# Kernel optimization log

Hardware: AMD Instinct MI355X
Metric: run time of the kernel (lower is better)

Reference implementation:

```python
import jax, jax.numpy as jnp
import numpy as np

B, T, C = 64, 256, 1024
N_HEAD, HEAD_SIZE, KV_RANK = 16, 64, 128
BLOCK_SIZE = 256


def setup_inputs() -> dict:
    key = jax.random.key(0)
    ks = jax.random.split(key, 5)
    HD = N_HEAD * HEAD_SIZE
    # weights stored (in, out) so y = x @ W  (equivalent to torch Linear x @ W.T)
    def init(k, shape):
        fan_in = shape[0]
        bound = 1.0 / np.sqrt(fan_in)
        return jax.random.uniform(k, shape, jnp.float32, -bound, bound)
    return {
        "x": jax.random.normal(ks[0], (B, T, C), jnp.float32),
        "w_kv_down": init(ks[1], (C, KV_RANK)),
        "w_kv_up": init(ks[2], (KV_RANK, 2 * HD)),
        "w_q": init(ks[3], (C, HD)),
        "w_out": init(ks[4], (HD, C)),
    }


def reference(x, w_kv_down, w_kv_up, w_q, w_out):
    Bx, Tx, Cx = x.shape
    HD = N_HEAD * HEAD_SIZE
    latent_kv = x @ w_kv_down                          # [B,T,r]
    kv = latent_kv @ w_kv_up                            # [B,T,2*H*D]
    k, v = kv[..., :HD], kv[..., HD:]
    k = k.reshape(Bx, Tx, N_HEAD, HEAD_SIZE)           # [B,T,H,D]
    v = v.reshape(Bx, Tx, N_HEAD, HEAD_SIZE)
    q = (x @ w_q).reshape(Bx, Tx, N_HEAD, HEAD_SIZE)
    scale = HEAD_SIZE ** -0.5
    att = jnp.einsum("bqhd,bkhd->bhqk", q, k) * scale  # [B,H,T,T]
    causal = jnp.tril(jnp.ones((Tx, Tx), dtype=bool))
    att = jnp.where(causal, att, -jnp.inf)
    att = jax.nn.softmax(att, axis=-1)                  # dropout = identity (eval)
    y = jnp.einsum("bhqk,bkhd->bqhd", att, v)          # [B,T,H,D]
    y = y.reshape(Bx, Tx, HD)
    return y @ w_out
```

## Files before the change

### kernel.cpp

```cpp
#include <hip/hip_runtime.h>
#include <hip/hip_bf16.h>
#include <cstdint>
#include <cstddef>

typedef short short8 __attribute__((ext_vector_type(8)));
typedef float floatx4 __attribute__((ext_vector_type(4)));
typedef float floatx16 __attribute__((ext_vector_type(16)));
typedef unsigned short u16;
typedef unsigned int u32;

__device__ __forceinline__ u16 f2bf(float f) {
    __hip_bfloat16 h = __float2bfloat16(f);
    return __builtin_bit_cast(u16, h);
}

__device__ __forceinline__ void gload_lds16(const void* g, void* l) {
    __builtin_amdgcn_global_load_lds(
        (const __attribute__((address_space(1))) void*)g,
        (__attribute__((address_space(3))) void*)l, 16, 0, 0);
}

__global__ __launch_bounds__(256) void prep(const float* __restrict__ x, u16* __restrict__ xb,
                                            const float* __restrict__ wq, const float* __restrict__ wkvd,
                                            const float* __restrict__ wkvu, const float* __restrict__ wo,
                                            u16* __restrict__ wql_t, u16* __restrict__ wkvu_t,
                                            u16* __restrict__ wo_t) {
    const int b = blockIdx.x;
    if (b < 2048) {
        const int n4 = 16384 * 1024 / 4;
        for (int i = b * 256 + threadIdx.x; i < n4; i += 2048 * 256) {
            float4 v = ((const float4*)x)[i];
            ushort4 o;
            o.x = f2bf(v.x); o.y = f2bf(v.y); o.z = f2bf(v.z); o.w = f2bf(v.w);
            ((ushort4*)xb)[i] = o;
        }
    } else {
        __shared__ float tile[32][33];
        const float* W; u16* Wt; int K, N, lb;
        if (b < 3072)      { W = wq;   Wt = wql_t;                       K = 1024; N = 1024; lb = b - 2048; }
        else if (b < 3200) { W = wkvd; Wt = wql_t + (size_t)1024 * 1024; K = 1024; N = 128;  lb = b - 3072; }
        else if (b < 3456) { W = wkvu; Wt = wkvu_t;                      K = 128;  N = 2048; lb = b - 3200; }
        else               { W = wo;   Wt = wo_t;                        K = 1024; N = 1024; lb = b - 3456; }
        const int nb = N / 32;
        const int n0 = (lb % nb) * 32, k0 = (lb / nb) * 32;
        const int tx = threadIdx.x & 31, ty = threadIdx.x >> 5;
        #pragma unroll
        for (int i = 0; i < 32; i += 8)
            tile[ty + i][tx] = W[(size_t)(k0 + ty + i) * N + n0 + tx];
        __syncthreads();
        #pragma unroll
        for (int i = 0; i < 32; i += 8)
            Wt[(size_t)(n0 + ty + i) * K + k0 + tx] = f2bf(tile[tx][ty + i]);
    }
}

template <int MODE>
__global__ __launch_bounds__(256, 4) void gemm_bt64(const u16* __restrict__ A, const u16* __restrict__ Bt,
                                                    void* __restrict__ C, int M, int N, int K, int ncols) {
    __shared__ __align__(16) u16 As[128 * 64];
    __shared__ __align__(16) u16 Bs[128 * 64];
    const int tid = threadIdx.x;
    const int lane = tid & 63, wid = tid >> 6;
    const int wr = wid >> 1, wc = wid & 1;
    const int l15 = lane & 15, hi = lane >> 4;

    const int nwg = gridDim.x, q8 = nwg >> 3;
    const int wg = (blockIdx.x & 7) * q8 + (blockIdx.x >> 3);
    const int m0 = (wg / ncols) * 128, n0 = (wg % ncols) * 128;

    const u16* Ab = A + (size_t)m0 * K;
    const u16* Bb = Bt + (size_t)n0 * K;

    u32 soff[4];
    #pragma unroll
    for (int l = 0; l < 4; l++) {
        int p = l * 256 + tid, c = p ^ ((p >> 3) & 7);
        soff[l] = (u32)((c >> 3) * K + (c & 7) * 8);
    }

    int afo[4][2], bfo[4][2];
    #pragma unroll
    for (int i = 0; i < 4; i++) {
        #pragma unroll
        for (int ks = 0; ks < 2; ks++) {
            int ra = wr * 64 + i * 16 + l15;
            afo[i][ks] = ((ra * 8 + ks * 4 + hi) ^ (ra & 7)) * 8;
            int rb = wc * 64 + i * 16 + l15;
            bfo[i][ks] = ((rb * 8 + ks * 4 + hi) ^ (rb & 7)) * 8;
        }
    }

    floatx4 acc[4][4] = {};

    for (int k0 = 0; k0 < K; k0 += 64) {
        #pragma unroll
        for (int l = 0; l < 4; l++)
            gload_lds16(Ab + soff[l] + k0, As + (size_t)(l * 256 + wid * 64) * 8);
        #pragma unroll
        for (int l = 0; l < 4; l++)
            gload_lds16(Bb + soff[l] + k0, Bs + (size_t)(l * 256 + wid * 64) * 8);
        __syncthreads();
        #pragma unroll
        for (int ks = 0; ks < 2; ks++) {
            short8 af[4], bf[4];
            #pragma unroll
            for (int i = 0; i < 4; i++) af[i] = *(const short8*)&As[afo[i][ks]];
            #pragma unroll
            for (int j = 0; j < 4; j++) bf[j] = *(const short8*)&Bs[bfo[j][ks]];
            #pragma unroll
            for (int i = 0; i < 4; i++) {
                #pragma unroll
                for (int j = 0; j < 4; j++)
                    acc[i][j] = __builtin_amdgcn_mfma_f32_16x16x32_bf16(af[i], bf[j], acc[i][j], 0, 0, 0);
            }
        }
        __syncthreads();
    }

    const int cr = hi * 4, cc = l15;
    #pragma unroll
    for (int i = 0; i < 4; i++) {
        #pragma unroll
        for (int j = 0; j < 4; j++) {
            int row = m0 + wr * 64 + i * 16 + cr;
            int col = n0 + wc * 64 + j * 16 + cc;
            #pragma unroll
            for (int r = 0; r < 4; r++) {
                float v = acc[i][j][r];
                int rr = row + r;
                if (MODE == 0) {
                    ((float*)C)[(size_t)rr * N + col] = v;
                } else {
                    if (col < 1024) {
                        int h = col >> 6, dd = col & 63;
                        ((u16*)C)[(((size_t)(rr >> 8) * 16 + h) * 256 + (rr & 255)) * 64 + dd] = f2bf(v);
                    } else {
                        u16* lat = (u16*)C + (size_t)16384 * 1024;
                        lat[(size_t)rr * 128 + (col - 1024)] = f2bf(v);
                    }
                }
            }
        }
    }
}

__global__ __launch_bounds__(256, 2) void attn_fused(const u16* __restrict__ Qh, const u16* __restrict__ Lat,
                                                     const u16* __restrict__ Wu, u16* __restrict__ Y) {
    constexpr int T = 256, HD = 1024;
    constexpr int VS = 264;
    __shared__ __align__(16) u16 Ks[256 * 64];
    __shared__ __align__(16) u16 Vt[64 * VS];

    const int tid = threadIdx.x, lane = tid & 63, wid = tid >> 6;
    const int bh = blockIdx.x;
    const int b = bh >> 4, h = bh & 15;
    const size_t base = (size_t)bh * (T * 64);
    const size_t baseY = (size_t)b * T * HD + (size_t)h * 64;

    const int qcol = lane & 31, hi2 = lane >> 5;

    {
        const u16* latb = Lat + (size_t)b * 256 * 128;
        const u16* wK = Wu + (size_t)(h * 64) * 128;
        const u16* wV = Wu + (size_t)(1024 + h * 64) * 128;

        #pragma unroll
        for (int i = 0; i < 4; i++) {
            const int tt = wid * 2 + (i >> 1), dt = i & 1;
            const u16* lp = &latb[(size_t)(tt * 32 + qcol) * 128 + hi2 * 8];
            const u16* kp = &wK[(size_t)(dt * 32 + qcol) * 128 + hi2 * 8];
            const u16* vp = &wV[(size_t)(dt * 32 + qcol) * 128 + hi2 * 8];
            floatx16 ck = {0}, cv = {0};
            #pragma unroll
            for (int ks = 0; ks < 8; ks++) {
                short8 lf = *(const short8*)&lp[ks * 16];
                short8 kf = *(const short8*)&kp[ks * 16];
                short8 vf = *(const short8*)&vp[ks * 16];
                ck = __builtin_amdgcn_mfma_f32_32x32x16_bf16(lf, kf, ck, 0, 0, 0);
                cv = __builtin_amdgcn_mfma_f32_32x32x16_bf16(vf, lf, cv, 0, 0, 0);
            }
            const int dK = dt * 32 + qcol;
            const int tV = tt * 32 + qcol;
            #pragma unroll
            for (int r = 0; r < 16; r++) {
                const int rloc = (r & 3) + 8 * (r >> 2) + 4 * hi2;
                const int t = tt * 32 + rloc;
                const int xt = (t & 7) ^ ((t >> 3) & 3);
                Ks[t * 64 + (((dK >> 3) ^ xt) << 3) + (dK & 7)] = f2bf(ck[r]);
                Vt[(dt * 32 + rloc) * VS + tV] = f2bf(cv[r]);
            }
        }
    }
    __syncthreads();

    const float c_exp = 0.125f * 1.44269504088896f;
    const u16* qbase = Qh + base;
    const u16* vrow0 = &Vt[qcol * VS];
    const u16* vrow1 = &Vt[(qcol + 32) * VS];

    #pragma unroll 1
    for (int half = 0; half < 2; half++) {
        const int qb = half ? (7 - wid) : wid;

        short8 qf[4];
        {
            const u16* qp = &qbase[(size_t)(qb * 32 + qcol) * 64 + hi2 * 8];
            #pragma unroll
            for (int i = 0; i < 4; i++) qf[i] = *(const short8*)&qp[i * 16];
        }

        floatx16 y0 = {0}, y1 = {0};
        float lsum = 0.f;

        for (int kt = 0; kt <= qb; kt++) {
            const int tK = kt * 32 + qcol;
            const int xt = (tK & 7) ^ ((tK >> 3) & 3);
            const u16* kp = &Ks[tK * 64];
            floatx16 s = {0};
            #pragma unroll
            for (int i = 0; i < 4; i++) {
                short8 kf = *(const short8*)&kp[((i * 2 + hi2) ^ xt) << 3];
                s = __builtin_amdgcn_mfma_f32_32x32x16_bf16(kf, qf[i], s, 0, 0, 0);
            }

            const bool diag = (kt == qb);
            u32 pk[8];
            #pragma unroll
            for (int r2 = 0; r2 < 8; r2++) {
                const int r0 = 2 * r2;
                const int kr0 = (r0 & 3) + 8 * (r0 >> 2) + 4 * hi2;
                float p0 = exp2f(s[r0] * c_exp);
                float p1 = exp2f(s[r0 + 1] * c_exp);
                if (diag) {
                    if (kr0 > qcol) p0 = 0.f;
                    if (kr0 + 1 > qcol) p1 = 0.f;
                }
                lsum += p0 + p1;
                pk[r2] = (u32)f2bf(p0) | ((u32)f2bf(p1) << 16);
            }

            #pragma unroll
            for (int kh2 = 0; kh2 < 2; kh2++) {
                u32 a0 = pk[kh2 * 4 + 0], a1 = pk[kh2 * 4 + 1];
                u32 b0 = pk[kh2 * 4 + 2], b1 = pk[kh2 * 4 + 3];
                asm volatile("v_permlane32_swap_b32 %0, %1" : "+v"(a0), "+v"(b0));
                asm volatile("v_permlane32_swap_b32 %0, %1" : "+v"(a1), "+v"(b1));
                int4 w;
                w.x = (int)a0; w.y = (int)a1; w.z = (int)b0; w.w = (int)b1;
                short8 pa = __builtin_bit_cast(short8, w);
                const int tofs = kt * 32 + kh2 * 16 + hi2 * 8;
                short8 vf0 = *(const short8*)&vrow0[tofs];
                short8 vf1 = *(const short8*)&vrow1[tofs];
                y0 = __builtin_amdgcn_mfma_f32_32x32x16_bf16(pa, vf0, y0, 0, 0, 0);
                y1 = __builtin_amdgcn_mfma_f32_32x32x16_bf16(pa, vf1, y1, 0, 0, 0);
            }
        }

        lsum += __shfl_xor(lsum, 32);
        const float linv = 1.0f / lsum;

        float sc[16];
        #pragma unroll
        for (int r = 0; r < 16; r++)
            sc[r] = __shfl(linv, (r & 3) + 8 * (r >> 2) + 4 * hi2, 64);

        #pragma unroll
        for (int r = 0; r < 16; r++) {
            const int qloc = (r & 3) + 8 * (r >> 2) + 4 * hi2;
            const size_t rowoff = baseY + (size_t)(qb * 32 + qloc) * HD;
            Y[rowoff + qcol]      = f2bf(y0[r] * sc[r]);
            Y[rowoff + 32 + qcol] = f2bf(y1[r] * sc[r]);
        }
    }
}

extern "C" void kernel_launch(void* const* d_in, const int* in_sizes, int n_in,
                              void* d_out, int out_size, void* d_ws, size_t ws_size,
                              hipStream_t stream) {
    const float* x         = (const float*)d_in[0];
    const float* w_kv_down = (const float*)d_in[1];
    const float* w_kv_up   = (const float*)d_in[2];
    const float* w_q       = (const float*)d_in[3];
    const float* w_out     = (const float*)d_in[4];
    float* out = (float*)d_out;

    constexpr int Bb = 64, Tt = 256, Cc = 1024, HD = 1024, R = 128;
    constexpr int M = Bb * Tt;

    char* ws = (char*)d_ws;
    auto alloc = [&](size_t bytes) {
        void* p = (void*)ws;
        ws += (bytes + 255) & ~(size_t)255;
        return p;
    };
    u16* xb      = (u16*)alloc((size_t)M * Cc * 2);
    u16* wql_t   = (u16*)alloc((size_t)(HD + R) * Cc * 2);
    u16* wkvu_t  = (u16*)alloc((size_t)2 * HD * R * 2);
    u16* wo_t    = (u16*)alloc((size_t)Cc * HD * 2);
    u16* qh      = (u16*)alloc((size_t)M * HD * 2);
    u16* latentb = (u16*)alloc((size_t)M * R * 2);
    u16* yb      = (u16*)alloc((size_t)M * HD * 2);

    prep<<<4480, 256, 0, stream>>>(x, xb, w_q, w_kv_down, w_kv_up, w_out, wql_t, wkvu_t, wo_t);

    gemm_bt64<4><<<dim3(128 * 9), 256, 0, stream>>>(xb, wql_t, qh, M, HD + R, Cc, 9);
    attn_fused<<<Bb * 16, 256, 0, stream>>>(qh, latentb, wkvu_t, yb);
    gemm_bt64<0><<<dim3(128 * 8), 256, 0, stream>>>(yb, wo_t, out, M, Cc, HD, 8);
}
```

Baseline: 175.0 us.

## Stage latent tile in LDS via async loads and reuse weight fragments

The latent tile is now copied into shared memory with global_load_lds using an XOR swizzle, and the K/V up-projection reads it from there. Loop order is restructured so each K/V weight fragment is loaded once per k-step and reused across two row tiles, which needs all eight accumulators live at once. Results are written to Ks/Vt after an extra barrier because that LDS region aliases the staged latent. This removes redundant global loads of weights and of the latent, at the cost of higher register pressure and an extra sync.

```diff
diff --git a/kernel.cpp b/kernel.cpp
--- a/kernel.cpp
+++ b/kernel.cpp
@@ -148,8 +148,9 @@
                                                      const u16* __restrict__ Wu, u16* __restrict__ Y) {
     constexpr int T = 256, HD = 1024;
     constexpr int VS = 264;
-    __shared__ __align__(16) u16 Ks[256 * 64];
-    __shared__ __align__(16) u16 Vt[64 * VS];
+    __shared__ __align__(16) u16 lds[33280];
+    u16* Ks = lds;
+    u16* Vt = lds + 16384;
 
     const int tid = threadIdx.x, lane = tid & 63, wid = tid >> 6;
     const int bh = blockIdx.x;
@@ -161,34 +162,54 @@
 
     {
         const u16* latb = Lat + (size_t)b * 256 * 128;
+        #pragma unroll
+        for (int l = 0; l < 16; l++) {
+            int p = l * 256 + tid;
+            int c = p ^ ((p >> 4) & 15);
+            gload_lds16(latb + (size_t)c * 8, lds + (size_t)(l * 256 + wid * 64) * 8);
+        }
+    }
+    __syncthreads();
+
+    floatx16 ck[4] = {}, cv[4] = {};
+    {
         const u16* wK = Wu + (size_t)(h * 64) * 128;
         const u16* wV = Wu + (size_t)(1024 + h * 64) * 128;
-
-        #pragma unroll
-        for (int i = 0; i < 4; i++) {
-            const int tt = wid * 2 + (i >> 1), dt = i & 1;
-            const u16* lp = &latb[(size_t)(tt * 32 + qcol) * 128 + hi2 * 8];
-            const u16* kp = &wK[(size_t)(dt * 32 + qcol) * 128 + hi2 * 8];
-            const u16* vp = &wV[(size_t)(dt * 32 + qcol) * 128 + hi2 * 8];
-            floatx16 ck = {0}, cv = {0};
-            #pragma unroll
-            for (int ks = 0; ks < 8; ks++) {
-                short8 lf = *(const short8*)&lp[ks * 16];
-                short8 kf = *(const short8*)&kp[ks * 16];
-                short8 vf = *(const short8*)&vp[ks * 16];
-                ck = __builtin_amdgcn_mfma_f32_32x32x16_bf16(lf, kf, ck, 0, 0, 0);
-                cv = __builtin_amdgcn_mfma_f32_32x32x16_bf16(vf, lf, cv, 0, 0, 0);
-            }
-            const int dK = dt * 32 + qcol;
-            const int tV = tt * 32 + qcol;
-            #pragma unroll
-            for (int r = 0; r < 16; r++) {
-                const int rloc = (r & 3) + 8 * (r >> 2) + 4 * hi2;
-                const int t = tt * 32 + rloc;
-                const int xt = (t & 7) ^ ((t >> 3) & 3);
-                Ks[t * 64 + (((dK >> 3) ^ xt) << 3) + (dK & 7)] = f2bf(ck[r]);
-                Vt[(dt * 32 + rloc) * VS + tV] = f2bf(cv[r]);
-            }
+        #pragma unroll
+        for (int ks = 0; ks < 8; ks++) {
+            short8 kf[2], vf[2];
+            #pragma unroll
+            for (int dt = 0; dt < 2; dt++) {
+                kf[dt] = *(const short8*)&wK[(size_t)(dt * 32 + qcol) * 128 + hi2 * 8 + ks * 16];
+                vf[dt] = *(const short8*)&wV[(size_t)(dt * 32 + qcol) * 128 + hi2 * 8 + ks * 16];
+            }
+            #pragma unroll
+            for (int it = 0; it < 2; it++) {
+                const int row = (wid * 2 + it) * 32 + qcol;
+                const int c = row * 16 + hi2 + 2 * ks;
+                short8 lf = *(const short8*)&lds[(size_t)(c ^ (row & 15)) * 8];
+                #pragma unroll
+                for (int dt = 0; dt < 2; dt++) {
+                    ck[it * 2 + dt] = __builtin_amdgcn_mfma_f32_32x32x16_bf16(lf, kf[dt], ck[it * 2 + dt], 0, 0, 0);
+                    cv[it * 2 + dt] = __builtin_amdgcn_mfma_f32_32x32x16_bf16(vf[dt], lf, cv[it * 2 + dt], 0, 0, 0);
+                }
+            }
+        }
+    }
+    __syncthreads();
+
+    #pragma unroll
+    for (int i = 0; i < 4; i++) {
+        const int tt = wid * 2 + (i >> 1), dt = i & 1;
+        const int dK = dt * 32 + qcol;
+        const int tV = tt * 32 + qcol;
+        #pragma unroll
+        for (int r = 0; r < 16; r++) {
+            const int rloc = (r & 3) + 8 * (r >> 2) + 4 * hi2;
+            const int t = tt * 32 + rloc;
+            const int xt = (t & 7) ^ ((t >> 3) & 3);
+            Ks[t * 64 + (((dK >> 3) ^ xt) << 3) + (dK & 7)] = f2bf(ck[i][r]);
+            Vt[(dt * 32 + rloc) * VS + tV] = f2bf(cv[i][r]);
         }
     }
     __syncthreads();
```

Measured after the change: 152.6 us (median of 2 runs). -12.8%, faster.
